# Performance work log

Measured on AMD Instinct MI355X. Metric: run time of the kernel, lower is better.

The kernel has to match this reference:

```python
import jax, jax.numpy as jnp
import numpy as np

B, CAP, H, NH = 128, 65536, 512, 8
HD = H // NH
GH = H // 4  # gate hidden


def setup_inputs() -> dict:
    key = jax.random.key(0)
    ks = jax.random.split(key, 8)
    s = 1.0 / np.sqrt(H)
    sg = 1.0 / np.sqrt(GH)
    return {
        "query": jax.random.normal(ks[0], (B, H), jnp.float32),
        "memory_keys": jax.random.normal(ks[1], (CAP, H), jnp.float32) * s,
        "memory_values": jax.random.normal(ks[2], (CAP, H), jnp.float32) * s,
        "in_proj_w": jax.random.normal(ks[3], (3 * H, H), jnp.float32) * s,
        "in_proj_b": jnp.zeros((3 * H,), jnp.float32),
        "out_proj_w": jax.random.normal(ks[4], (H, H), jnp.float32) * s,
        "out_proj_b": jnp.zeros((H,), jnp.float32),
        "gate_w1": jax.random.normal(ks[5], (GH, H), jnp.float32) * s,
        "gate_b1": jnp.zeros((GH,), jnp.float32),
        "gate_w2": jax.random.normal(ks[6], (1, GH), jnp.float32) * sg,
        "gate_b2": jnp.zeros((1,), jnp.float32),
        "usage_count": jnp.zeros((CAP,), jnp.float32),
        "last_used": jnp.zeros((CAP,), jnp.float32),
        "step_counter": 1,
    }


def reference(query, memory_keys, memory_values, in_proj_w, in_proj_b,
              out_proj_w, out_proj_b, gate_w1, gate_b1, gate_w2, gate_b2,
              usage_count, last_used, step_counter):
    # nn.MultiheadAttention packed projections: rows [0:H]=Wq, [H:2H]=Wk, [2H:3H]=Wv
    wq, wk, wv = in_proj_w[:H], in_proj_w[H:2 * H], in_proj_w[2 * H:]
    bq, bk, bv = in_proj_b[:H], in_proj_b[H:2 * H], in_proj_b[2 * H:]

    q = (query @ wq.T + bq).reshape(B, NH, HD)           # [B, h, d] (q_len = 1)
    k = (memory_keys @ wk.T + bk).reshape(CAP, NH, HD)   # [C, h, d]
    v = (memory_values @ wv.T + bv).reshape(CAP, NH, HD)  # [C, h, d]

    scores = jnp.einsum('bhd,chd->bhc', q, k) / np.sqrt(HD)  # [B, h, C]
    attn = jax.nn.softmax(scores, axis=-1)
    ctx = jnp.einsum('bhc,chd->bhd', attn, v).reshape(B, H)
    attn_out = ctx @ out_proj_w.T + out_proj_b               # [B, H]

    # usage bookkeeping: attn_weights averaged over heads, then over batch
    avg_attn = attn.mean(axis=(0, 1))                        # [C]
    new_usage = usage_count + avg_attn
    new_last = jnp.where(avg_attn > 1e-3,
                         jnp.float32(step_counter), last_used)

    # gating MLP: Linear -> ReLU -> Linear -> Sigmoid
    gate = jax.nn.sigmoid(
        jax.nn.relu(query @ gate_w1.T + gate_b1) @ gate_w2.T + gate_b2)  # [B, 1]
    memory_output = gate * attn_out                          # [B, H]
    return memory_output, new_usage, new_last
```

## Files before the change

kernel.cpp:

```cpp
#include <hip/hip_runtime.h>
#include <stdint.h>


typedef __bf16 b16x8 __attribute__((ext_vector_type(8)));
typedef float f32x4 __attribute__((ext_vector_type(4)));
typedef unsigned short u16x8 __attribute__((ext_vector_type(8)));

static __device__ __forceinline__ unsigned short f2bf(float f) {
  unsigned int u = __float_as_uint(f);
  u = (u + 0x7FFFu + ((u >> 16) & 1u)) >> 16;
  return (unsigned short)u;
}

static __device__ __forceinline__ f32x4 MFMA(b16x8 a, b16x8 b, f32x4 c) {
  return __builtin_amdgcn_mfma_f32_16x16x32_bf16(a, b, c, 0, 0, 0);
}

#define GLL16(g, l)                                                          \
  __builtin_amdgcn_global_load_lds(                                          \
      (const __attribute__((address_space(1))) void*)(g),                    \
      (__attribute__((address_space(3))) void*)(l), 16, 0, 0)

__global__ void k_convert_w(const float* __restrict__ w, unsigned short* __restrict__ dst) {
  int i = blockIdx.x * 256 + threadIdx.x;
  float4 v = reinterpret_cast<const float4*>(w + 512 * 512)[i];
  ushort4 o;
  o.x = f2bf(v.x); o.y = f2bf(v.y); o.z = f2bf(v.z); o.w = f2bf(v.w);
  reinterpret_cast<ushort4*>(dst)[i] = o;
}

__global__ void k_proj_q(const float* __restrict__ query, const float* __restrict__ w,
                         const float* __restrict__ bias, unsigned short* __restrict__ qout) {
  __shared__ float qs[512];
  int b = blockIdx.x, j = threadIdx.x;
  qs[j] = query[b * 512 + j];
  __syncthreads();
  float acc = bias[j];
  const float4* q4 = reinterpret_cast<const float4*>(qs);
  const float4* w4 = reinterpret_cast<const float4*>(w + j * 512);
#pragma unroll 8
  for (int i = 0; i < 128; ++i) {
    float4 a = q4[i], c = w4[i];
    acc += a.x * c.x + a.y * c.y + a.z * c.z + a.w * c.w;
  }
  qout[b * 512 + j] = f2bf(acc);
}

__global__ void k_gate(const float* __restrict__ query, const float* __restrict__ w1,
                       const float* __restrict__ b1, const float* __restrict__ w2,
                       const float* __restrict__ b2, float* __restrict__ gate) {
  __shared__ float qs[512];
  __shared__ float red[2];
  int b = blockIdx.x, j = threadIdx.x;
  qs[j] = query[b * 512 + j];
  qs[j + 128] = query[b * 512 + j + 128];
  qs[j + 256] = query[b * 512 + j + 256];
  qs[j + 384] = query[b * 512 + j + 384];
  __syncthreads();
  float acc = b1[j];
  const float4* q4 = reinterpret_cast<const float4*>(qs);
  const float4* w4 = reinterpret_cast<const float4*>(w1 + j * 512);
#pragma unroll 8
  for (int i = 0; i < 128; ++i) {
    float4 a = q4[i], c = w4[i];
    acc += a.x * c.x + a.y * c.y + a.z * c.z + a.w * c.w;
  }
  float t = fmaxf(acc, 0.f) * w2[j];
#pragma unroll
  for (int off = 1; off < 64; off <<= 1) t += __shfl_xor(t, off, 64);
  if ((j & 63) == 0) red[j >> 6] = t;
  __syncthreads();
  if (j == 0) {
    float z = red[0] + red[1] + b2[0];
    gate[b] = 1.f / (1.f + __builtin_amdgcn_exp2f(-z * 1.44269504088896f));
  }
}

__global__ __launch_bounds__(256) void k_proj_kv(
    const float* __restrict__ mk, const float* __restrict__ mv,
    const unsigned short* __restrict__ wkb, const unsigned short* __restrict__ wvb,
    const float* __restrict__ in_b,
    unsigned short* __restrict__ kout, unsigned short* __restrict__ vtout) {
  const int isV = blockIdx.z;
  const float* Ag = isV ? mv : mk;
  const unsigned short* W = isV ? wvb : wkb;
  const float* bias = in_b + (isV ? 1024 : 512);
  const int j0 = blockIdx.x * 128;
  const int c0 = blockIdx.y * 128;
  const int tid = threadIdx.x;
  const int wv = tid >> 6, wr = wv >> 1, wc = wv & 1;
  const int ln = tid & 15, g = (tid & 63) >> 4;
  const int sw = (ln >> 1) & 3;

  __shared__ __align__(16) unsigned short Al[128 * 32];
  __shared__ __align__(16) unsigned short Wl[128 * 32];

  f32x4 acc[4][4];
#pragma unroll
  for (int m = 0; m < 4; ++m)
#pragma unroll
    for (int n = 0; n < 4; ++n) acc[m][n] = {0.f, 0.f, 0.f, 0.f};

  const int arow = tid >> 1, ah = tid & 1;
  const float* aptr = Ag + (size_t)(c0 + arow) * 512 + ah * 16;
  const int s_a = (arow >> 1) & 3;
  unsigned short* awr0 = &Al[arow * 32 + (((2 * ah) ^ s_a) << 3)];
  unsigned short* awr1 = &Al[arow * 32 + (((2 * ah + 1) ^ s_a) << 3)];

  const int r0 = tid >> 2, p0 = (tid & 3) ^ ((r0 >> 1) & 3);
  const int r1 = 64 + (tid >> 2), p1 = (tid & 3) ^ ((r1 >> 1) & 3);
  const unsigned short* wsrc0 = W + (size_t)(j0 + r0) * 512 + p0 * 8;
  const unsigned short* wsrc1 = W + (size_t)(j0 + r1) * 512 + p1 * 8;
  unsigned short* wdst0 = &Wl[(wv << 6) * 8];
  unsigned short* wdst1 = &Wl[(256 + (wv << 6)) * 8];

  for (int kk = 0; kk < 16; ++kk) {
    GLL16(wsrc0 + kk * 32, wdst0);
    GLL16(wsrc1 + kk * 32, wdst1);
    const float4* ap = reinterpret_cast<const float4*>(aptr + kk * 32);
    float4 f0 = ap[0], f1 = ap[1], f2 = ap[2], f3 = ap[3];
    u16x8 lo, hi;
    lo[0] = f2bf(f0.x); lo[1] = f2bf(f0.y); lo[2] = f2bf(f0.z); lo[3] = f2bf(f0.w);
    lo[4] = f2bf(f1.x); lo[5] = f2bf(f1.y); lo[6] = f2bf(f1.z); lo[7] = f2bf(f1.w);
    hi[0] = f2bf(f2.x); hi[1] = f2bf(f2.y); hi[2] = f2bf(f2.z); hi[3] = f2bf(f2.w);
    hi[4] = f2bf(f3.x); hi[5] = f2bf(f3.y); hi[6] = f2bf(f3.z); hi[7] = f2bf(f3.w);
    *reinterpret_cast<u16x8*>(awr0) = lo;
    *reinterpret_cast<u16x8*>(awr1) = hi;
    __syncthreads();

    b16x8 af[4], wf[4];
#pragma unroll
    for (int m = 0; m < 4; ++m) {
      int row = 64 * wr + 16 * m + ln;
      af[m] = *reinterpret_cast<const b16x8*>(&Al[row * 32 + ((g ^ sw) << 3)]);
    }
#pragma unroll
    for (int n = 0; n < 4; ++n) {
      int row = 64 * wc + 16 * n + ln;
      wf[n] = *reinterpret_cast<const b16x8*>(&Wl[row * 32 + ((g ^ sw) << 3)]);
    }
#pragma unroll
    for (int m = 0; m < 4; ++m)
#pragma unroll
      for (int n = 0; n < 4; ++n) acc[m][n] = MFMA(af[m], wf[n], acc[m][n]);
    __syncthreads();
  }

  float bj[4];
#pragma unroll
  for (int n = 0; n < 4; ++n) bj[n] = bias[j0 + 64 * wc + 16 * n + ln];
#pragma unroll
  for (int m = 0; m < 4; ++m)
#pragma unroll
    for (int n = 0; n < 4; ++n) {
      int j = j0 + 64 * wc + 16 * n + ln;
      if (!isV) {
#pragma unroll
        for (int r = 0; r < 4; ++r) {
          int c = c0 + 64 * wr + 16 * m + 4 * g + r;
          kout[(size_t)c * 512 + j] = f2bf(acc[m][n][r] + bj[n]);
        }
      } else {
        ushort4 o;
        o.x = f2bf(acc[m][n][0] + bj[n]);
        o.y = f2bf(acc[m][n][1] + bj[n]);
        o.z = f2bf(acc[m][n][2] + bj[n]);
        o.w = f2bf(acc[m][n][3] + bj[n]);
        int c = c0 + 64 * wr + 16 * m + 4 * g;
        *reinterpret_cast<ushort4*>(&vtout[(size_t)j * 65536 + c]) = o;
      }
    }
}

__global__ __launch_bounds__(256) void k_attn1(
    const unsigned short* __restrict__ kb, const unsigned short* __restrict__ vt,
    const unsigned short* __restrict__ qb,
    float* __restrict__ l_ws, float* __restrict__ ctxT) {
  const int h = blockIdx.y, cg = blockIdx.x;
  const int tid = threadIdx.x;
  const int wv = tid >> 6, wr = wv >> 1, wc = wv & 1;
  const int ln = tid & 15, g = (tid & 63) >> 4;
  __shared__ __align__(16) unsigned short kS[128 * 64];
  __shared__ __align__(16) unsigned short pS[128 * 128];
  __shared__ __align__(16) unsigned short vS[64 * 128];
  const float SC = 0.125f * 1.44269504088896f;

  b16x8 qf[4][2];
#pragma unroll
  for (int n = 0; n < 4; ++n)
#pragma unroll
    for (int ks = 0; ks < 2; ++ks) {
      int b = 64 * wc + 16 * n + ln;
      qf[n][ks] = *reinterpret_cast<const b16x8*>(&qb[(size_t)b * 512 + h * 64 + ks * 32 + g * 8]);
    }
  f32x4 pacc[2][4];
#pragma unroll
  for (int m = 0; m < 2; ++m)
#pragma unroll
    for (int n = 0; n < 4; ++n) pacc[m][n] = {0.f, 0.f, 0.f, 0.f};
  float lsum[4] = {0.f, 0.f, 0.f, 0.f};

  for (int it = 0; it < 8; ++it) {
    int c0g = cg * 1024 + it * 128;
#pragma unroll
    for (int i = 0; i < 4; ++i) {
      int fl = i * 256 + tid, row = fl >> 3, p8 = fl & 7;
      uint4 d = *reinterpret_cast<const uint4*>(&kb[(size_t)(c0g + row) * 512 + h * 64 + p8 * 8]);
      *reinterpret_cast<uint4*>(&kS[(row * 8 + (p8 ^ (row & 7))) * 8]) = d;
    }
#pragma unroll
    for (int i = 0; i < 4; ++i) {
      int fl = i * 256 + tid, row = fl >> 4, p16 = fl & 15;
      uint4 d = *reinterpret_cast<const uint4*>(&vt[(size_t)(h * 64 + row) * 65536 + c0g + p16 * 8]);
      *reinterpret_cast<uint4*>(&vS[(row * 16 + (p16 ^ (row & 7))) * 8]) = d;
    }
    __syncthreads();

    f32x4 sacc[4][4];
#pragma unroll
    for (int m = 0; m < 4; ++m)
#pragma unroll
      for (int n = 0; n < 4; ++n) sacc[m][n] = {0.f, 0.f, 0.f, 0.f};
#pragma unroll
    for (int ks = 0; ks < 2; ++ks) {
      b16x8 a[4];
#pragma unroll
      for (int m = 0; m < 4; ++m) {
        int row = 64 * wr + 16 * m + ln;
        a[m] = *reinterpret_cast<const b16x8*>(&kS[(row * 8 + ((ks * 4 + g) ^ (row & 7))) * 8]);
      }
#pragma unroll
      for (int m = 0; m < 4; ++m)
#pragma unroll
        for (int n = 0; n < 4; ++n) sacc[m][n] = MFMA(a[m], qf[n][ks], sacc[m][n]);
    }
#pragma unroll
    for (int m = 0; m < 4; ++m)
#pragma unroll
      for (int n = 0; n < 4; ++n) {
        float p0 = __builtin_amdgcn_exp2f(sacc[m][n][0] * SC);
        float p1 = __builtin_amdgcn_exp2f(sacc[m][n][1] * SC);
        float p2 = __builtin_amdgcn_exp2f(sacc[m][n][2] * SC);
        float p3 = __builtin_amdgcn_exp2f(sacc[m][n][3] * SC);
        lsum[n] += (p0 + p1) + (p2 + p3);
        int b = 64 * wc + 16 * n + ln;
        int c = 64 * wr + 16 * m + 4 * g;
        int base = b * 128 + (((c >> 3) ^ (b & 7)) * 8) + (c & 7);
        ushort2 lo, hi;
        lo.x = f2bf(p0); lo.y = f2bf(p1);
        hi.x = f2bf(p2); hi.y = f2bf(p3);
        *reinterpret_cast<ushort2*>(&pS[base]) = lo;
        *reinterpret_cast<ushort2*>(&pS[base + 2]) = hi;
      }
    __syncthreads();
#pragma unroll
    for (int ks = 0; ks < 4; ++ks) {
      b16x8 av[2], bp[4];
#pragma unroll
      for (int m = 0; m < 2; ++m) {
        int row = 32 * wr + 16 * m + ln;
        av[m] = *reinterpret_cast<const b16x8*>(&vS[(row * 16 + ((ks * 4 + g) ^ (row & 7))) * 8]);
      }
#pragma unroll
      for (int n = 0; n < 4; ++n) {
        int row = 64 * wc + 16 * n + ln;
        bp[n] = *reinterpret_cast<const b16x8*>(&pS[(row * 16 + ((ks * 4 + g) ^ (row & 7))) * 8]);
      }
#pragma unroll
      for (int m = 0; m < 2; ++m)
#pragma unroll
        for (int n = 0; n < 4; ++n) pacc[m][n] = MFMA(av[m], bp[n], pacc[m][n]);
    }
    __syncthreads();
  }
#pragma unroll
  for (int n = 0; n < 4; ++n) {
    float v = lsum[n];
    v += __shfl_xor(v, 16, 64);
    v += __shfl_xor(v, 32, 64);
    if ((tid & 63) < 16) atomicAdd(&l_ws[h * 128 + 64 * wc + 16 * n + ln], v);
  }
#pragma unroll
  for (int m = 0; m < 2; ++m)
#pragma unroll
    for (int n = 0; n < 4; ++n)
#pragma unroll
      for (int r = 0; r < 4; ++r) {
        int d = 32 * wr + 16 * m + 4 * g + r;
        int b = 64 * wc + 16 * n + ln;
        atomicAdd(&ctxT[(h * 64 + d) * 128 + b], pacc[m][n][r]);
      }
}

__global__ __launch_bounds__(256) void k_attn2(
    const unsigned short* __restrict__ kb, const unsigned short* __restrict__ qb,
    const float* __restrict__ l_ws, float* __restrict__ avgA) {
  const int h = blockIdx.y, cg = blockIdx.x;
  const int tid = threadIdx.x;
  const int wv = tid >> 6, wr = wv >> 1, wc = wv & 1;
  const int ln = tid & 15, g = (tid & 63) >> 4;
  __shared__ __align__(16) unsigned short kS[128 * 64];
  __shared__ float wS[128];
  const float SC = 0.125f * 1.44269504088896f;
  if (tid < 128) wS[tid] = 1.f / l_ws[h * 128 + tid];
  b16x8 qf[4][2];
#pragma unroll
  for (int n = 0; n < 4; ++n)
#pragma unroll
    for (int ks = 0; ks < 2; ++ks) {
      int b = 64 * wc + 16 * n + ln;
      qf[n][ks] = *reinterpret_cast<const b16x8*>(&qb[(size_t)b * 512 + h * 64 + ks * 32 + g * 8]);
    }
  __syncthreads();
  float wn[4];
#pragma unroll
  for (int n = 0; n < 4; ++n) wn[n] = wS[64 * wc + 16 * n + ln];

  for (int it = 0; it < 8; ++it) {
    int c0g = cg * 1024 + it * 128;
#pragma unroll
    for (int i = 0; i < 4; ++i) {
      int fl = i * 256 + tid, row = fl >> 3, p8 = fl & 7;
      uint4 d = *reinterpret_cast<const uint4*>(&kb[(size_t)(c0g + row) * 512 + h * 64 + p8 * 8]);
      *reinterpret_cast<uint4*>(&kS[(row * 8 + (p8 ^ (row & 7))) * 8]) = d;
    }
    __syncthreads();
    f32x4 sacc[4][4];
#pragma unroll
    for (int m = 0; m < 4; ++m)
#pragma unroll
      for (int n = 0; n < 4; ++n) sacc[m][n] = {0.f, 0.f, 0.f, 0.f};
#pragma unroll
    for (int ks = 0; ks < 2; ++ks) {
      b16x8 a[4];
#pragma unroll
      for (int m = 0; m < 4; ++m) {
        int row = 64 * wr + 16 * m + ln;
        a[m] = *reinterpret_cast<const b16x8*>(&kS[(row * 8 + ((ks * 4 + g) ^ (row & 7))) * 8]);
      }
#pragma unroll
      for (int m = 0; m < 4; ++m)
#pragma unroll
        for (int n = 0; n < 4; ++n) sacc[m][n] = MFMA(a[m], qf[n][ks], sacc[m][n]);
    }
#pragma unroll
    for (int m = 0; m < 4; ++m) {
      float s0 = 0.f, s1 = 0.f, s2 = 0.f, s3 = 0.f;
#pragma unroll
      for (int n = 0; n < 4; ++n) {
        s0 += __builtin_amdgcn_exp2f(sacc[m][n][0] * SC) * wn[n];
        s1 += __builtin_amdgcn_exp2f(sacc[m][n][1] * SC) * wn[n];
        s2 += __builtin_amdgcn_exp2f(sacc[m][n][2] * SC) * wn[n];
        s3 += __builtin_amdgcn_exp2f(sacc[m][n][3] * SC) * wn[n];
      }
#pragma unroll
      for (int off = 1; off < 16; off <<= 1) {
        s0 += __shfl_xor(s0, off, 64);
        s1 += __shfl_xor(s1, off, 64);
        s2 += __shfl_xor(s2, off, 64);
        s3 += __shfl_xor(s3, off, 64);
      }
      if (ln == 0) {
        int c = c0g + 64 * wr + 16 * m + 4 * g;
        atomicAdd(&avgA[c], s0);
        atomicAdd(&avgA[c + 1], s1);
        atomicAdd(&avgA[c + 2], s2);
        atomicAdd(&avgA[c + 3], s3);
      }
    }
    __syncthreads();
  }
}

__global__ void k_finalize(const float* __restrict__ ctxT, const float* __restrict__ l_ws,
                           const float* __restrict__ wout, const float* __restrict__ bout,
                           const float* __restrict__ gate, float* __restrict__ out) {
  __shared__ float cs[512];
  int b = blockIdx.x, j = threadIdx.x;
  cs[j] = ctxT[j * 128 + b] / l_ws[(j >> 6) * 128 + b];
  __syncthreads();
  float acc = bout[j];
  const float4* c4 = reinterpret_cast<const float4*>(cs);
  const float4* w4 = reinterpret_cast<const float4*>(wout + j * 512);
#pragma unroll 8
  for (int i = 0; i < 128; ++i) {
    float4 a = c4[i], c = w4[i];
    acc += a.x * c.x + a.y * c.y + a.z * c.z + a.w * c.w;
  }
  out[b * 512 + j] = gate[b] * acc;
}

__global__ void k_usage(const float* __restrict__ avgA, const float* __restrict__ usage,
                        const float* __restrict__ last, const int* __restrict__ step,
                        float* __restrict__ out_usage, float* __restrict__ out_last) {
  int c = blockIdx.x * 256 + threadIdx.x;
  float avg = avgA[c] * (1.f / 1024.f);
  out_usage[c] = usage[c] + avg;
  out_last[c] = (avg > 0.001f) ? (float)step[0] : last[c];
}

extern "C" void kernel_launch(void* const* d_in, const int* in_sizes, int n_in,
                              void* d_out, int out_size, void* d_ws, size_t ws_size,
                              hipStream_t stream) {
  const float* query = (const float*)d_in[0];
  const float* mk    = (const float*)d_in[1];
  const float* mv    = (const float*)d_in[2];
  const float* in_w  = (const float*)d_in[3];
  const float* in_b  = (const float*)d_in[4];
  const float* out_w = (const float*)d_in[5];
  const float* out_b = (const float*)d_in[6];
  const float* gw1   = (const float*)d_in[7];
  const float* gb1   = (const float*)d_in[8];
  const float* gw2   = (const float*)d_in[9];
  const float* gb2   = (const float*)d_in[10];
  const float* usage = (const float*)d_in[11];
  const float* last  = (const float*)d_in[12];
  const int*   step  = (const int*)d_in[13];

  char* ws = (char*)d_ws;
  unsigned short* qb  = (unsigned short*)(ws);
  unsigned short* wkb = (unsigned short*)(ws + 131072);
  unsigned short* wvb = (unsigned short*)(ws + 655360);
  unsigned short* kb  = (unsigned short*)(ws + 1179648);
  unsigned short* vt  = (unsigned short*)(ws + 68288512);
  float* l_ws = (float*)(ws + 135397376);
  float* ctxT = (float*)(ws + 135401472);
  float* avgA = (float*)(ws + 135663616);
  float* gate = (float*)(ws + 135925760);
  float* out = (float*)d_out;

  hipMemsetAsync(ws + 135397376, 0, 4096 + 262144 + 262144, stream);

  k_convert_w<<<512, 256, 0, stream>>>(in_w, wkb);
  k_proj_q<<<128, 512, 0, stream>>>(query, in_w, in_b, qb);
  k_gate<<<128, 128, 0, stream>>>(query, gw1, gb1, gw2, gb2, gate);
  k_proj_kv<<<dim3(4, 512, 2), 256, 0, stream>>>(mk, mv, wkb, wvb, in_b, kb, vt);
  k_attn1<<<dim3(64, 8), 256, 0, stream>>>(kb, vt, qb, l_ws, ctxT);
  k_attn2<<<dim3(64, 8), 256, 0, stream>>>(kb, qb, l_ws, avgA);
  k_finalize<<<128, 512, 0, stream>>>(ctxT, l_ws, out_w, out_b, gate, out);
  k_usage<<<256, 256, 0, stream>>>(avgA, usage, last, step, out + 65536, out + 131072);
}
```

Before: 414.1 us.

## Double-buffer K/V projection LDS tiles and remap blocks for XCD locality

The K/V projection GEMM now keeps two LDS buffers, so the next k-slice's global loads (A as fp32 through registers, W through global_load_lds) are issued before the MFMAs on the current slice. That halves the barriers per iteration and hides load latency behind compute. The grid is flattened to 1D and remapped so that blocks sharing the same A rows and weights land on the same XCD, which should improve L2 reuse. The bf16 conversion now uses the native __bf16 cast instead of manual rounding. LDS use doubles.

```diff
diff --git a/kernel.cpp b/kernel.cpp
--- a/kernel.cpp
+++ b/kernel.cpp
@@ -4,12 +4,9 @@
 
 typedef __bf16 b16x8 __attribute__((ext_vector_type(8)));
 typedef float f32x4 __attribute__((ext_vector_type(4)));
-typedef unsigned short u16x8 __attribute__((ext_vector_type(8)));
 
 static __device__ __forceinline__ unsigned short f2bf(float f) {
-  unsigned int u = __float_as_uint(f);
-  u = (u + 0x7FFFu + ((u >> 16) & 1u)) >> 16;
-  return (unsigned short)u;
+  return __builtin_bit_cast(unsigned short, (__bf16)f);
 }
 
 static __device__ __forceinline__ f32x4 MFMA(b16x8 a, b16x8 b, f32x4 c) {
@@ -81,19 +78,21 @@
     const unsigned short* __restrict__ wkb, const unsigned short* __restrict__ wvb,
     const float* __restrict__ in_b,
     unsigned short* __restrict__ kout, unsigned short* __restrict__ vtout) {
-  const int isV = blockIdx.z;
+  const int p = blockIdx.x;
+  const int xcd = p & 7, slot = p >> 3;
+  const int isV = xcd >> 2;
+  const int j0 = (slot & 3) * 128;
+  const int c0 = ((xcd & 3) * 128 + (slot >> 2)) * 128;
   const float* Ag = isV ? mv : mk;
   const unsigned short* W = isV ? wvb : wkb;
   const float* bias = in_b + (isV ? 1024 : 512);
-  const int j0 = blockIdx.x * 128;
-  const int c0 = blockIdx.y * 128;
   const int tid = threadIdx.x;
   const int wv = tid >> 6, wr = wv >> 1, wc = wv & 1;
   const int ln = tid & 15, g = (tid & 63) >> 4;
   const int sw = (ln >> 1) & 3;
 
-  __shared__ __align__(16) unsigned short Al[128 * 32];
-  __shared__ __align__(16) unsigned short Wl[128 * 32];
+  __shared__ __align__(16) unsigned short Al[2][128 * 32];
+  __shared__ __align__(16) unsigned short Wl[2][128 * 32];
 
   f32x4 acc[4][4];
 #pragma unroll
@@ -104,45 +103,65 @@
   const int arow = tid >> 1, ah = tid & 1;
   const float* aptr = Ag + (size_t)(c0 + arow) * 512 + ah * 16;
   const int s_a = (arow >> 1) & 3;
-  unsigned short* awr0 = &Al[arow * 32 + (((2 * ah) ^ s_a) << 3)];
-  unsigned short* awr1 = &Al[arow * 32 + (((2 * ah + 1) ^ s_a) << 3)];
+  const int aoff0 = arow * 32 + (((2 * ah) ^ s_a) << 3);
+  const int aoff1 = arow * 32 + (((2 * ah + 1) ^ s_a) << 3);
 
   const int r0 = tid >> 2, p0 = (tid & 3) ^ ((r0 >> 1) & 3);
   const int r1 = 64 + (tid >> 2), p1 = (tid & 3) ^ ((r1 >> 1) & 3);
   const unsigned short* wsrc0 = W + (size_t)(j0 + r0) * 512 + p0 * 8;
   const unsigned short* wsrc1 = W + (size_t)(j0 + r1) * 512 + p1 * 8;
-  unsigned short* wdst0 = &Wl[(wv << 6) * 8];
-  unsigned short* wdst1 = &Wl[(256 + (wv << 6)) * 8];
-
+  const int wdoff0 = (wv << 6) * 8;
+  const int wdoff1 = (256 + (wv << 6)) * 8;
+
+  {
+    GLL16(wsrc0, &Wl[0][wdoff0]);
+    GLL16(wsrc1, &Wl[0][wdoff1]);
+    const float4* ap = reinterpret_cast<const float4*>(aptr);
+    float4 g0 = ap[0], g1 = ap[1], g2 = ap[2], g3 = ap[3];
+    b16x8 lo, hi;
+    lo[0] = (__bf16)g0.x; lo[1] = (__bf16)g0.y; lo[2] = (__bf16)g0.z; lo[3] = (__bf16)g0.w;
+    lo[4] = (__bf16)g1.x; lo[5] = (__bf16)g1.y; lo[6] = (__bf16)g1.z; lo[7] = (__bf16)g1.w;
+    hi[0] = (__bf16)g2.x; hi[1] = (__bf16)g2.y; hi[2] = (__bf16)g2.z; hi[3] = (__bf16)g2.w;
+    hi[4] = (__bf16)g3.x; hi[5] = (__bf16)g3.y; hi[6] = (__bf16)g3.z; hi[7] = (__bf16)g3.w;
+    *reinterpret_cast<b16x8*>(&Al[0][aoff0]) = lo;
+    *reinterpret_cast<b16x8*>(&Al[0][aoff1]) = hi;
+  }
+  __syncthreads();
+
+#pragma unroll 2
   for (int kk = 0; kk < 16; ++kk) {
-    GLL16(wsrc0 + kk * 32, wdst0);
-    GLL16(wsrc1 + kk * 32, wdst1);
-    const float4* ap = reinterpret_cast<const float4*>(aptr + kk * 32);
-    float4 f0 = ap[0], f1 = ap[1], f2 = ap[2], f3 = ap[3];
-    u16x8 lo, hi;
-    lo[0] = f2bf(f0.x); lo[1] = f2bf(f0.y); lo[2] = f2bf(f0.z); lo[3] = f2bf(f0.w);
-    lo[4] = f2bf(f1.x); lo[5] = f2bf(f1.y); lo[6] = f2bf(f1.z); lo[7] = f2bf(f1.w);
-    hi[0] = f2bf(f2.x); hi[1] = f2bf(f2.y); hi[2] = f2bf(f2.z); hi[3] = f2bf(f2.w);
-    hi[4] = f2bf(f3.x); hi[5] = f2bf(f3.y); hi[6] = f2bf(f3.z); hi[7] = f2bf(f3.w);
-    *reinterpret_cast<u16x8*>(awr0) = lo;
-    *reinterpret_cast<u16x8*>(awr1) = hi;
-    __syncthreads();
-
+    const int cur = kk & 1, nxt = cur ^ 1;
+    float4 g0, g1, g2, g3;
+    if (kk < 15) {
+      const float4* ap = reinterpret_cast<const float4*>(aptr + (kk + 1) * 32);
+      g0 = ap[0]; g1 = ap[1]; g2 = ap[2]; g3 = ap[3];
+      GLL16(wsrc0 + (kk + 1) * 32, &Wl[nxt][wdoff0]);
+      GLL16(wsrc1 + (kk + 1) * 32, &Wl[nxt][wdoff1]);
+    }
     b16x8 af[4], wf[4];
 #pragma unroll
     for (int m = 0; m < 4; ++m) {
       int row = 64 * wr + 16 * m + ln;
-      af[m] = *reinterpret_cast<const b16x8*>(&Al[row * 32 + ((g ^ sw) << 3)]);
+      af[m] = *reinterpret_cast<const b16x8*>(&Al[cur][row * 32 + ((g ^ sw) << 3)]);
     }
 #pragma unroll
     for (int n = 0; n < 4; ++n) {
       int row = 64 * wc + 16 * n + ln;
-      wf[n] = *reinterpret_cast<const b16x8*>(&Wl[row * 32 + ((g ^ sw) << 3)]);
+      wf[n] = *reinterpret_cast<const b16x8*>(&Wl[cur][row * 32 + ((g ^ sw) << 3)]);
     }
 #pragma unroll
     for (int m = 0; m < 4; ++m)
 #pragma unroll
       for (int n = 0; n < 4; ++n) acc[m][n] = MFMA(af[m], wf[n], acc[m][n]);
+    if (kk < 15) {
+      b16x8 lo, hi;
+      lo[0] = (__bf16)g0.x; lo[1] = (__bf16)g0.y; lo[2] = (__bf16)g0.z; lo[3] = (__bf16)g0.w;
+      lo[4] = (__bf16)g1.x; lo[5] = (__bf16)g1.y; lo[6] = (__bf16)g1.z; lo[7] = (__bf16)g1.w;
+      hi[0] = (__bf16)g2.x; hi[1] = (__bf16)g2.y; hi[2] = (__bf16)g2.z; hi[3] = (__bf16)g2.w;
+      hi[4] = (__bf16)g3.x; hi[5] = (__bf16)g3.y; hi[6] = (__bf16)g3.z; hi[7] = (__bf16)g3.w;
+      *reinterpret_cast<b16x8*>(&Al[nxt][aoff0]) = lo;
+      *reinterpret_cast<b16x8*>(&Al[nxt][aoff1]) = hi;
+    }
     __syncthreads();
   }
 
@@ -434,7 +453,7 @@
   k_convert_w<<<512, 256, 0, stream>>>(in_w, wkb);
   k_proj_q<<<128, 512, 0, stream>>>(query, in_w, in_b, qb);
   k_gate<<<128, 128, 0, stream>>>(query, gw1, gb1, gw2, gb2, gate);
-  k_proj_kv<<<dim3(4, 512, 2), 256, 0, stream>>>(mk, mv, wkb, wvb, in_b, kb, vt);
+  k_proj_kv<<<4096, 256, 0, stream>>>(mk, mv, wkb, wvb, in_b, kb, vt);
   k_attn1<<<dim3(64, 8), 256, 0, stream>>>(kb, vt, qb, l_ws, ctxT);
   k_attn2<<<dim3(64, 8), 256, 0, stream>>>(kb, qb, l_ws, avgA);
   k_finalize<<<128, 512, 0, stream>>>(ctxT, l_ws, out_w, out_b, gate, out);
```

Result: faster. 391.7 us (-5.4%).
